# Kernel tuning notes

Measured on AMD Instinct MI355X. Metric: run time of the kernel, lower is better.

The kernel has to match this reference:

```python
import jax, jax.numpy as jnp
import numpy as np

N_OUT = 4096
N_IN = 4096
TOKENS = 8192
BITWIDTH = 4
GROUP_SIZE = 128
ZERO = 2 ** (BITWIDTH - 1)  # symmetric GPTQ zero-point


def setup_inputs() -> dict:
    key = jax.random.key(0)
    kx, kq, ks = jax.random.split(key, 3)
    x = jax.random.normal(kx, (TOKENS, N_IN), dtype=jnp.float32)
    qweight = jax.random.randint(kq, (N_OUT, N_IN), 0, 2 ** BITWIDTH, dtype=jnp.int32)
    scales = jax.random.uniform(ks, (N_OUT, N_IN // GROUP_SIZE), dtype=jnp.float32) * 0.02 + 0.001
    return {"x": x, "qweight": qweight, "scales": scales}


def reference(x, qweight, scales):
    # Dequantize: W[o, i] = (q[o, i] - zero) * scales[o, i // group_size]
    q = qweight.astype(x.dtype) - jnp.asarray(ZERO, dtype=x.dtype)
    # reshape input dim into (n_groups, group_size) and broadcast group scales
    qg = q.reshape(N_OUT, N_IN // GROUP_SIZE, GROUP_SIZE)
    w = (qg * scales[:, :, None].astype(x.dtype)).reshape(N_OUT, N_IN)
    # out = x @ W^T  -> [tokens, n_out]
    return jnp.einsum('ti,oi->to', x, w)
```

## Files before the change

### kernel.cpp

```cpp
#include <hip/hip_runtime.h>
#include <hip/hip_bf16.h>
#include <stdint.h>

#define TOKENS_C 8192
#define NIN_C    4096
#define NOUT_C   4096
#define GROUP_C  128
#define QZERO_C  8

typedef float   f32x4  __attribute__((ext_vector_type(4)));
typedef int     i32x4  __attribute__((ext_vector_type(4)));

#define GAS __attribute__((address_space(1)))
#define LAS __attribute__((address_space(3)))

__device__ __forceinline__ void gload16(const void* g, void* l) {
  __builtin_amdgcn_global_load_lds((const GAS void*)g, (LAS void*)l, 16, 0, 0);
}

__global__ __launch_bounds__(256) void quant_x_kernel(
    const float* __restrict__ x, char* __restrict__ x8, float* __restrict__ sx)
{
  const int t   = blockIdx.x;
  const int tid = threadIdx.x;
  const float* xr = x + (size_t)t * NIN_C;
  f32x4 v[4];
#pragma unroll
  for (int r = 0; r < 4; ++r) v[r] = *(const f32x4*)(xr + tid * 16 + r * 4);
  float m = 0.f;
#pragma unroll
  for (int r = 0; r < 4; ++r)
#pragma unroll
    for (int e = 0; e < 4; ++e) m = fmaxf(m, fabsf(v[r][e]));
#pragma unroll
  for (int off = 32; off >= 1; off >>= 1) m = fmaxf(m, __shfl_xor(m, off));
  __shared__ float wmax[4];
  if ((tid & 63) == 0) wmax[tid >> 6] = m;
  __syncthreads();
  m = fmaxf(fmaxf(wmax[0], wmax[1]), fmaxf(wmax[2], wmax[3]));
  m = fmaxf(m, 1e-20f);
  const float inv = 127.0f / m;
  if (tid == 0) sx[t] = m / 127.0f;
  i32x4 o;
#pragma unroll
  for (int r = 0; r < 4; ++r) {
    int q0 = (int)rintf(v[r][0] * inv), q1 = (int)rintf(v[r][1] * inv);
    int q2 = (int)rintf(v[r][2] * inv), q3 = (int)rintf(v[r][3] * inv);
    o[r] = (q0 & 255) | ((q1 & 255) << 8) | ((q2 & 255) << 16) | ((q3 & 255) << 24);
  }
  *(i32x4*)(x8 + (size_t)t * NIN_C + tid * 16) = o;
}

__global__ __launch_bounds__(256) void repack_w_kernel(
    const int* __restrict__ qw, char* __restrict__ w8)
{
  const size_t base = ((size_t)blockIdx.x * 256 + threadIdx.x) * 16;
  i32x4 o;
#pragma unroll
  for (int r = 0; r < 4; ++r) {
    i32x4 q = *(const i32x4*)(qw + base + r * 4);
    o[r] = ((q[0] - QZERO_C) & 255) | (((q[1] - QZERO_C) & 255) << 8) |
           (((q[2] - QZERO_C) & 255) << 16) | (((q[3] - QZERO_C) & 255) << 24);
  }
  *(i32x4*)(w8 + base) = o;
}

__global__ __launch_bounds__(256) void tsc_kernel(
    const float* __restrict__ sc, float* __restrict__ sT)
{
  const int id = blockIdx.x * 256 + threadIdx.x;
  const int o = id & (NOUT_C - 1), g = id >> 12;
  sT[id] = sc[o * (NIN_C / GROUP_C) + g];
}

#define BM 256
#define BN 256
#define BKB 64
#define NT (NIN_C / BKB)

__global__ __launch_bounds__(1024) void gemm_i8_kernel(
    const char* __restrict__ Ag,
    const char* __restrict__ Bg,
    const float* __restrict__ sTg,
    const float* __restrict__ sx,
    float* __restrict__ C)
{
  constexpr int N = NOUT_C, KB = NIN_C;
  __shared__ char smem[131072];

  const int tid  = threadIdx.x;
  const int lane = tid & 63;
  const int wid  = tid >> 6;
  const int wm   = wid >> 2;
  const int wn   = wid & 3;
  const int bm   = blockIdx.x;
  const int bn   = blockIdx.y;

  const int frow  = lane & 15;
  const int klane = lane >> 4;

  const int gsrc = ((tid & 3) ^ ((tid >> 3) & 3)) * 16;
  const uint32_t aoff = (uint32_t)((bm * BM + (tid >> 2)) * KB + gsrc);
  const uint32_t boff = (uint32_t)((bn * BN + (tid >> 2)) * KB + gsrc);
  const int sdst = tid * 16;

#define STG(tt, SW) { char* d_ = smem + (SW) * 32768 + sdst;                   \
    gload16(Ag + aoff + (uint32_t)(tt) * BKB, d_);                             \
    gload16(Bg + boff + (uint32_t)(tt) * BKB, d_ + 16384); }

  const int ccol0 = bn * BN + wn * 64;
  const int scoff = ccol0 + frow;
#define LD_S(dst, g)                                                           \
  _Pragma("unroll")                                                            \
  for (int j_ = 0; j_ < 4; ++j_)                                               \
    dst[j_] = sTg[(size_t)(g) * NOUT_C + scoff + j_ * 16];

  const int kswz = (klane ^ ((frow >> 1) & 3)) << 4;
  const int ard0 = (wm * 64 + frow) * 64 + kswz;
  const int brd0 = (wn * 64 + frow) * 64 + kswz + 16384;

  f32x4 facc[4][4] = {};
  const i32x4 zq = {0, 0, 0, 0};

#define MFI(a_, b_, c_) __builtin_amdgcn_mfma_i32_16x16x64_i8(a_, b_, c_, 0, 0, 0)
#define APPLY(ii, jj, pv, scur)                                                \
  { f32x4 tf_;                                                                 \
    tf_[0] = (float)(pv)[0]; tf_[1] = (float)(pv)[1];                          \
    tf_[2] = (float)(pv)[2]; tf_[3] = (float)(pv)[3];                          \
    facc[ii][jj] += tf_ * (scur)[jj]; }
#define BAR __builtin_amdgcn_s_barrier()
#define WAITV(n) asm volatile("s_waitcnt vmcnt(" #n ")" ::: "memory")
#define SBAR0 __builtin_amdgcn_sched_barrier(0)

#define TILE(tt, SLOT, scur, DO_LDS, snxt, gnxt, DO_STG, WVN)                  \
  {                                                                            \
    const char* As_ = smem + (SLOT) * 32768;                                   \
    const char* Bs_ = smem + (SLOT) * 32768;                                   \
    if (DO_LDS) { LD_S(snxt, gnxt); }                                          \
    if (DO_STG) { STG((tt) + 3, ((SLOT) + 3) & 3); }                           \
    i32x4 bf0 = *(const i32x4*)(Bs_ + brd0);                                   \
    i32x4 bf1 = *(const i32x4*)(Bs_ + brd0 + 1024);                            \
    i32x4 bf2 = *(const i32x4*)(Bs_ + brd0 + 2048);                            \
    i32x4 bf3 = *(const i32x4*)(Bs_ + brd0 + 3072);                            \
    _Pragma("unroll")                                                          \
    for (int ii = 0; ii < 4; ++ii) {                                           \
      i32x4 ak = *(const i32x4*)(As_ + ard0 + ii * 1024);                      \
      i32x4 p0, p1, p2, p3;                                                    \
      __builtin_amdgcn_s_setprio(1);                                           \
      p0 = MFI(ak, bf0, zq); p1 = MFI(ak, bf1, zq);                            \
      p2 = MFI(ak, bf2, zq); p3 = MFI(ak, bf3, zq);                            \
      __builtin_amdgcn_s_setprio(0);                                           \
      APPLY(ii, 0, p0, scur); APPLY(ii, 1, p1, scur);                          \
      APPLY(ii, 2, p2, scur); APPLY(ii, 3, p3, scur);                          \
    }                                                                          \
    WAITV(WVN); SBAR0; BAR;                                                    \
  }

  float sA[4], sB[4];

  LD_S(sA, 0);
  SBAR0;
  STG(0, 0); STG(1, 1); STG(2, 2);
  WAITV(4);
  BAR; SBAR0;

  for (int t0 = 0; t0 < NT - 8; t0 += 4) {
    const int g0 = t0 >> 1;
    TILE(t0,     0, sA, 1, sB, g0 + 1, 1, 8);
    TILE(t0 + 1, 1, sA, 0, sB, 0,      1, 4);
    TILE(t0 + 2, 2, sB, 1, sA, g0 + 2, 1, 8);
    TILE(t0 + 3, 3, sB, 0, sA, 0,      1, 4);
  }
  TILE(56, 0, sA, 1, sB, 29, 1, 8);
  TILE(57, 1, sA, 0, sB, 0,  1, 4);
  TILE(58, 2, sB, 1, sA, 30, 1, 8);
  TILE(59, 3, sB, 0, sA, 0,  1, 4);
  TILE(60, 0, sA, 1, sB, 31, 1, 8);
  TILE(61, 1, sA, 0, sB, 0,  0, 2);
  TILE(62, 2, sB, 0, sA, 0,  0, 0);
  TILE(63, 3, sB, 0, sA, 0,  0, 0);

  const int crow0 = bm * BM + wm * 64;
  const int r0 = klane << 2;
  char* const wb0 = smem + wid * 4096;
  char* const wb1 = smem + 65536 + wid * 4096;
#pragma unroll
  for (int fi = 0; fi < 4; ++fi) {
    char* wb = (fi & 1) ? wb1 : wb0;
    const f32x4 sxv = *(const f32x4*)(sx + crow0 + fi * 16 + r0);
#pragma unroll
    for (int j = 0; j < 4; ++j) {
      f32x4 v = facc[fi][j];
#pragma unroll
      for (int r = 0; r < 4; ++r)
        *(float*)(wb + (r0 + r) * 256 + (j * 16 + frow) * 4) = v[r] * sxv[r];
    }
    __syncthreads();
#pragma unroll
    for (int sub = 0; sub < 4; ++sub) {
      const int row16 = klane + sub * 4;
      f32x4 v = *(const f32x4*)(wb + row16 * 256 + frow * 16);
      *(f32x4*)(C + (int64_t)(crow0 + fi * 16 + row16) * N + ccol0 + frow * 4) = v;
    }
  }
#undef STG
#undef LD_S
#undef MFI
#undef APPLY
#undef TILE
#undef BAR
#undef WAITV
#undef SBAR0
}

__global__ __launch_bounds__(256) void naive_kernel(
    const float* __restrict__ x, const int* __restrict__ qw,
    const float* __restrict__ sc, float* __restrict__ out)
{
  const int64_t idx = (int64_t)blockIdx.x * 256 + threadIdx.x;
  const int tok = (int)(idx >> 12);
  const int o   = (int)(idx & 4095);
  const float* xr = x + (int64_t)tok * NIN_C;
  const int* qr = qw + (int64_t)o * NIN_C;
  float acc = 0.f;
  for (int g = 0; g < NIN_C / GROUP_C; ++g) {
    float s = sc[(o << 5) | g];
    float ga = 0.f;
#pragma unroll 4
    for (int i = g * GROUP_C; i < (g + 1) * GROUP_C; ++i)
      ga += xr[i] * (float)(qr[i] - QZERO_C);
    acc += s * ga;
  }
  out[idx] = acc;
}

extern "C" void kernel_launch(void* const* d_in, const int* in_sizes, int n_in,
                              void* d_out, int out_size, void* d_ws, size_t ws_size,
                              hipStream_t stream) {
  const float* x  = (const float*)d_in[0];
  const int*   qw = (const int*)d_in[1];
  const float* sc = (const float*)d_in[2];
  float* out = (float*)d_out;

  const size_t x8_bytes = (size_t)TOKENS_C * NIN_C;
  const size_t w8_bytes = (size_t)NOUT_C * NIN_C;
  const size_t sx_bytes = (size_t)TOKENS_C * sizeof(float);
  const size_t sT_bytes = (size_t)(NIN_C / GROUP_C) * NOUT_C * sizeof(float);

  if (ws_size < x8_bytes + w8_bytes + sx_bytes + sT_bytes) {
    const int64_t total = (int64_t)TOKENS_C * NOUT_C;
    naive_kernel<<<(int)(total / 256), 256, 0, stream>>>(x, qw, sc, out);
    return;
  }

  char*  x8 = (char*)d_ws;
  char*  w8 = (char*)d_ws + x8_bytes;
  float* sx = (float*)((char*)d_ws + x8_bytes + w8_bytes);
  float* sT = (float*)((char*)d_ws + x8_bytes + w8_bytes + sx_bytes);

  quant_x_kernel<<<TOKENS_C, 256, 0, stream>>>(x, x8, sx);
  repack_w_kernel<<<(int)(w8_bytes / 16 / 256), 256, 0, stream>>>(qw, w8);
  tsc_kernel<<<(int)((NIN_C / GROUP_C) * NOUT_C / 256), 256, 0, stream>>>(sc, sT);
  {
    dim3 grid(TOKENS_C / BM, NOUT_C / BN);
    gemm_i8_kernel<<<grid, 1024, 0, stream>>>(x8, w8, sT, sx, out);
  }
}
```

Baseline: 330.6 us.

## Shrink int8 GEMM pipeline from four-stage to double-buffered LDS

Cuts the LDS ring from four 32KB stages to two, so each tile stages only the next tile and waits for all outstanding loads (vmcnt 0) before the barrier. It also removes the s_setprio around the MFMA bursts and makes the epilogue reuse a single LDS staging buffer, adding a barrier after each chunk. Halving shared memory could allow two 1024-thread blocks per CU, but prefetch depth drops to one tile and every tile now waits on a full drain, which exposes global load latency.

```diff
diff --git a/kernel.cpp b/kernel.cpp
--- a/kernel.cpp
+++ b/kernel.cpp
@@ -86,7 +86,7 @@
     float* __restrict__ C)
 {
   constexpr int N = NOUT_C, KB = NIN_C;
-  __shared__ char smem[131072];
+  __shared__ char smem[65536];
 
   const int tid  = threadIdx.x;
   const int lane = tid & 63;
@@ -132,12 +132,12 @@
 #define WAITV(n) asm volatile("s_waitcnt vmcnt(" #n ")" ::: "memory")
 #define SBAR0 __builtin_amdgcn_sched_barrier(0)
 
-#define TILE(tt, SLOT, scur, DO_LDS, snxt, gnxt, DO_STG, WVN)                  \
+#define TILE(tt, SLOT, scur, DO_LDS, snxt, gnxt, DO_STG)                       \
   {                                                                            \
     const char* As_ = smem + (SLOT) * 32768;                                   \
     const char* Bs_ = smem + (SLOT) * 32768;                                   \
     if (DO_LDS) { LD_S(snxt, gnxt); }                                          \
-    if (DO_STG) { STG((tt) + 3, ((SLOT) + 3) & 3); }                           \
+    if (DO_STG) { STG((tt) + 1, (SLOT) ^ 1); }                                 \
     i32x4 bf0 = *(const i32x4*)(Bs_ + brd0);                                   \
     i32x4 bf1 = *(const i32x4*)(Bs_ + brd0 + 1024);                            \
     i32x4 bf2 = *(const i32x4*)(Bs_ + brd0 + 2048);                            \
@@ -146,47 +146,42 @@
     for (int ii = 0; ii < 4; ++ii) {                                           \
       i32x4 ak = *(const i32x4*)(As_ + ard0 + ii * 1024);                      \
       i32x4 p0, p1, p2, p3;                                                    \
-      __builtin_amdgcn_s_setprio(1);                                           \
       p0 = MFI(ak, bf0, zq); p1 = MFI(ak, bf1, zq);                            \
       p2 = MFI(ak, bf2, zq); p3 = MFI(ak, bf3, zq);                            \
-      __builtin_amdgcn_s_setprio(0);                                           \
       APPLY(ii, 0, p0, scur); APPLY(ii, 1, p1, scur);                          \
       APPLY(ii, 2, p2, scur); APPLY(ii, 3, p3, scur);                          \
     }                                                                          \
-    WAITV(WVN); SBAR0; BAR;                                                    \
+    WAITV(0); SBAR0; BAR;                                                      \
   }
 
   float sA[4], sB[4];
 
   LD_S(sA, 0);
-  SBAR0;
-  STG(0, 0); STG(1, 1); STG(2, 2);
-  WAITV(4);
+  STG(0, 0);
+  WAITV(0);
   BAR; SBAR0;
 
-  for (int t0 = 0; t0 < NT - 8; t0 += 4) {
+  for (int t0 = 0; t0 < 56; t0 += 4) {
     const int g0 = t0 >> 1;
-    TILE(t0,     0, sA, 1, sB, g0 + 1, 1, 8);
-    TILE(t0 + 1, 1, sA, 0, sB, 0,      1, 4);
-    TILE(t0 + 2, 2, sB, 1, sA, g0 + 2, 1, 8);
-    TILE(t0 + 3, 3, sB, 0, sA, 0,      1, 4);
-  }
-  TILE(56, 0, sA, 1, sB, 29, 1, 8);
-  TILE(57, 1, sA, 0, sB, 0,  1, 4);
-  TILE(58, 2, sB, 1, sA, 30, 1, 8);
-  TILE(59, 3, sB, 0, sA, 0,  1, 4);
-  TILE(60, 0, sA, 1, sB, 31, 1, 8);
-  TILE(61, 1, sA, 0, sB, 0,  0, 2);
-  TILE(62, 2, sB, 0, sA, 0,  0, 0);
-  TILE(63, 3, sB, 0, sA, 0,  0, 0);
+    TILE(t0,     0, sA, 1, sB, g0 + 1, 1);
+    TILE(t0 + 1, 1, sA, 0, sB, 0,      1);
+    TILE(t0 + 2, 0, sB, 1, sA, g0 + 2, 1);
+    TILE(t0 + 3, 1, sB, 0, sA, 0,      1);
+  }
+  TILE(56, 0, sA, 1, sB, 29, 1);
+  TILE(57, 1, sA, 0, sB, 0,  1);
+  TILE(58, 0, sB, 1, sA, 30, 1);
+  TILE(59, 1, sB, 0, sA, 0,  1);
+  TILE(60, 0, sA, 1, sB, 31, 1);
+  TILE(61, 1, sA, 0, sB, 0,  1);
+  TILE(62, 0, sB, 0, sA, 0,  1);
+  TILE(63, 1, sB, 0, sA, 0,  0);
 
   const int crow0 = bm * BM + wm * 64;
   const int r0 = klane << 2;
-  char* const wb0 = smem + wid * 4096;
-  char* const wb1 = smem + 65536 + wid * 4096;
+  char* const wb = smem + wid * 4096;
 #pragma unroll
   for (int fi = 0; fi < 4; ++fi) {
-    char* wb = (fi & 1) ? wb1 : wb0;
     const f32x4 sxv = *(const f32x4*)(sx + crow0 + fi * 16 + r0);
 #pragma unroll
     for (int j = 0; j < 4; ++j) {
@@ -202,6 +197,7 @@
       f32x4 v = *(const f32x4*)(wb + row16 * 256 + frow * 16);
       *(f32x4*)(C + (int64_t)(crow0 + fi * 16 + row16) * N + ccol0 + frow * 4) = v;
     }
+    __syncthreads();
   }
 #undef STG
 #undef LD_S
```

Measured after the change: 280.5 us. 1.18x faster.
